# Performance work log

Measured on AMD Instinct MI355X. Metric: run time of the kernel, lower is better.

## Reference

```python
import jax, jax.numpy as jnp
import numpy as np

B, T, I, H, C = 1024, 256, 14, 128, 1


def setup_inputs() -> dict:
    key = jax.random.key(0)
    ks = jax.random.split(key, 12)
    s = 1.0 / np.sqrt(H)  # torch nn.LSTM / nn.Linear uniform init bound
    u = lambda k, shp: jax.random.uniform(k, shp, jnp.float32, -s, s)
    return {
        "x": jax.random.normal(ks[0], (B, T, I), jnp.float32),
        # layer 0 (input_size -> hidden), gate order i,f,g,o stacked along first dim (4H)
        "w_ih0": u(ks[1], (4 * H, I)), "w_hh0": u(ks[2], (4 * H, H)),
        "b_ih0": u(ks[3], (4 * H,)), "b_hh0": u(ks[4], (4 * H,)),
        # layer 1 (hidden -> hidden)
        "w_ih1": u(ks[5], (4 * H, H)), "w_hh1": u(ks[6], (4 * H, H)),
        "b_ih1": u(ks[7], (4 * H,)), "b_hh1": u(ks[8], (4 * H,)),
        # final linear head
        "w_lin": u(ks[9], (C, H)), "b_lin": u(ks[10], (C,)),
    }


def _lstm_layer(x_seq, w_ih, w_hh, b_ih, b_hh):
    """Single LSTM layer, batch_first input [B,T,D] -> hidden sequence [B,T,H]."""
    Bb = x_seq.shape[0]
    Hh = w_hh.shape[1]
    # Hoist the input projection out of the recurrence: one big GEMM over all timesteps.
    x_proj = jnp.einsum('btd,gd->btg', x_seq, w_ih) + b_ih + b_hh  # [B,T,4H]
    x_proj = jnp.swapaxes(x_proj, 0, 1)  # [T,B,4H] for scan over time
    h0 = jnp.zeros((Bb, Hh), x_seq.dtype)
    c0 = jnp.zeros((Bb, Hh), x_seq.dtype)

    def step(carry, xp):
        h, c = carry
        gates = xp + h @ w_hh.T  # [B,4H]
        i, f, g, o = jnp.split(gates, 4, axis=-1)  # torch gate order: i,f,g,o
        i = jax.nn.sigmoid(i)
        f = jax.nn.sigmoid(f)
        g = jnp.tanh(g)
        o = jax.nn.sigmoid(o)
        c = f * c + i * g
        h = o * jnp.tanh(c)
        return (h, c), h

    _, hs = jax.lax.scan(step, (h0, c0), x_proj)  # hs: [T,B,H]
    return jnp.swapaxes(hs, 0, 1)  # [B,T,H]


def reference(x, w_ih0, w_hh0, b_ih0, b_hh0, w_ih1, w_hh1, b_ih1, b_hh1, w_lin, b_lin):
    h1 = _lstm_layer(x, w_ih0, w_hh0, b_ih0, b_hh0)
    # nn.LSTM dropout=0.1 applies between layers only in training mode; inference => identity
    h2 = _lstm_layer(h1, w_ih1, w_hh1, b_ih1, b_hh1)
    last = h2[:, -1, :]  # [B,H] final timestep
    return last @ w_lin.T + b_lin  # [B,1]
```

## Files before the change

### kernel.cpp

```cpp
#include <hip/hip_runtime.h>

typedef _Float16 half8 __attribute__((ext_vector_type(8)));
typedef float floatx4 __attribute__((ext_vector_type(4)));

#define T_STEPS 256
#define BB      16
#define NTH     512
#define RING_W  16

#define WHH0_H  0
#define WIH1_H  65536
#define WHH1_H  131072
#define WIH0_H  196608
#define RING_H  229376
#define FLAG_B  4653056
#define FLAG_BYTES 16384

__device__ __forceinline__ float sig_(float z)  { return __builtin_amdgcn_rcpf(1.f + __expf(-z)); }
__device__ __forceinline__ float tanh_(float z) { return 1.f - 2.f * __builtin_amdgcn_rcpf(1.f + __expf(2.f * z)); }

__global__ __launch_bounds__(256) void prep_weights(
    const float* __restrict__ w_ih0, const float* __restrict__ w_hh0,
    const float* __restrict__ w_ih1, const float* __restrict__ w_hh1,
    _Float16* __restrict__ wf)
{
    const int idx = blockIdx.x * 256 + threadIdx.x;
    const int l  = idx & 63;
    const int ks = (idx >> 6) & 3;
    const int gi = (idx >> 8) & 3;
    const int wv = (idx >> 10) & 7;
    const int row = gi * 128 + wv * 16 + (l & 15);
    const int kb  = ks * 32 + (l >> 4) * 8;
#pragma unroll
    for (int j = 0; j < 8; ++j) {
        wf[WHH0_H + idx * 8 + j] = (_Float16)w_hh0[row * 128 + kb + j];
        wf[WIH1_H + idx * 8 + j] = (_Float16)w_ih1[row * 128 + kb + j];
        wf[WHH1_H + idx * 8 + j] = (_Float16)w_hh1[row * 128 + kb + j];
    }
    if (ks == 0) {
        const int lk = l >> 4;
        const int oi = ((wv * 4 + gi) * 64 + l) * 8;
#pragma unroll
        for (int j = 0; j < 8; ++j) {
            float v = 0.f;
            if (lk == 0)                v = w_ih0[row * 14 + j];
            else if (lk == 1 && j >= 2) v = w_ih0[row * 14 + 6 + j];
            wf[WIH0_H + oi + j] = (_Float16)v;
        }
    }
}

__global__ __launch_bounds__(NTH) void lstm2_pipe(
    const float* __restrict__ x, const _Float16* __restrict__ wf,
    const float* __restrict__ b_ih0, const float* __restrict__ b_hh0,
    const float* __restrict__ b_ih1, const float* __restrict__ b_hh1,
    const float* __restrict__ w_lin, const float* __restrict__ b_lin,
    float* __restrict__ out, char* __restrict__ wsb)
{
    __shared__ __align__(16) _Float16 hbuf[2][BB * 128];

    const int tid  = threadIdx.x;
    const int l    = tid & 63;
    const int wv   = tid >> 6;
    const int lrow = l & 15;
    const int lk   = l >> 4;
    const int bid  = blockIdx.x;
    const int pos  = bid & 7;
    const int role = (bid >> 3) & 1;
    const int g    = (bid >> 4) * 8 + pos;
    const int b0   = g * BB;

    _Float16* ring = (_Float16*)wsb + RING_H + (size_t)g * RING_W * 2048;
    int* flag_p = (int*)(wsb + FLAG_B) + g * 64;
    int* flag_c = flag_p + 32;

    for (int i = tid; i < 1024; i += NTH) ((unsigned*)hbuf[1])[i] = 0u;

    const half8* wsf = (const half8*)wf;

    if (role == 0) {
        half8 whh0f[16], wih0f[4];
#pragma unroll
        for (int gi = 0; gi < 4; ++gi) {
#pragma unroll
            for (int ks = 0; ks < 4; ++ks)
                whh0f[gi * 4 + ks] = wsf[WHH0_H / 8 + ((wv * 4 + gi) * 4 + ks) * 64 + l];
            wih0f[gi] = wsf[WIH0_H / 8 + (wv * 4 + gi) * 64 + l];
        }
        float bias1[4];
#pragma unroll
        for (int gi = 0; gi < 4; ++gi) {
            const int col = gi * 128 + wv * 16 + lrow;
            bias1[gi] = b_ih0[col] + b_hh0[col];
        }
        float c1[4] = {0.f, 0.f, 0.f, 0.f};

        const int coff = (lk == 1) ? 6 : 0;
        const float* xp = x + (size_t)(b0 + lrow) * (T_STEPS * 14) + coff;
        float xr[8];
#pragma unroll
        for (int j = 0; j < 8; ++j) xr[j] = xp[j];
        int seen_c = 0;
        __syncthreads();

        for (int t = 0; t < T_STEPS; ++t) {
            const int cur = t & 1, prv = cur ^ 1;
            half8 xh;
#pragma unroll
            for (int j = 0; j < 8; ++j) xh[j] = (_Float16)xr[j];
            if (t + 1 < T_STEPS) {
#pragma unroll
                for (int j = 0; j < 8; ++j) xr[j] = xp[(t + 1) * 14 + j];
            }
            const char* hrd = (const char*)hbuf[prv];
            half8 h1p[4];
#pragma unroll
            for (int ks = 0; ks < 4; ++ks) {
                const int off = lrow * 256 + ((ks * 64 + lk * 16) ^ ((lrow & 7) << 4));
                h1p[ks] = *(const half8*)(hrd + off);
            }
            floatx4 acc[4];
#pragma unroll
            for (int gi = 0; gi < 4; ++gi) {
                acc[gi] = (floatx4){bias1[gi], bias1[gi], bias1[gi], bias1[gi]};
                acc[gi] = __builtin_amdgcn_mfma_f32_16x16x32_f16(xh, wih0f[gi], acc[gi], 0, 0, 0);
#pragma unroll
                for (int ks = 0; ks < 4; ++ks)
                    acc[gi] = __builtin_amdgcn_mfma_f32_16x16x32_f16(h1p[ks], whh0f[gi * 4 + ks], acc[gi], 0, 0, 0);
            }
            if (t >= RING_W && tid == 0) {
                while (seen_c < t - (RING_W - 1)) {
                    seen_c = __hip_atomic_load(flag_c, __ATOMIC_RELAXED, __HIP_MEMORY_SCOPE_AGENT);
                    if (seen_c < t - (RING_W - 1)) __builtin_amdgcn_s_sleep(2);
                }
            }
            __syncthreads();
            char* hwr = (char*)hbuf[cur];
            _Float16* rt = ring + (size_t)(t & (RING_W - 1)) * 2048;
            const int u = wv * 16 + lrow;
#pragma unroll
            for (int r = 0; r < 4; ++r) {
                const float ig = sig_(acc[0][r]);
                const float fg = sig_(acc[1][r]);
                const float gg = tanh_(acc[2][r]);
                const float og = sig_(acc[3][r]);
                c1[r] = fg * c1[r] + ig * gg;
                const float hv = og * tanh_(c1[r]);
                const int b = lk * 4 + r;
                const _Float16 hh = (_Float16)hv;
                *(_Float16*)(hwr + b * 256 + ((u * 2) ^ ((b & 7) << 4))) = hh;
                rt[b * 128 + u] = hh;
            }
            __syncthreads();
            if (tid == 0)
                __hip_atomic_store(flag_p, t + 1, __ATOMIC_RELEASE, __HIP_MEMORY_SCOPE_AGENT);
        }
    } else {
        half8 wih1f[16], whh1f[16];
#pragma unroll
        for (int gi = 0; gi < 4; ++gi)
#pragma unroll
            for (int ks = 0; ks < 4; ++ks) {
                const int idx = ((wv * 4 + gi) * 4 + ks) * 64 + l;
                wih1f[gi * 4 + ks] = wsf[WIH1_H / 8 + idx];
                whh1f[gi * 4 + ks] = wsf[WHH1_H / 8 + idx];
            }
        float bias2[4];
#pragma unroll
        for (int gi = 0; gi < 4; ++gi) {
            const int col = gi * 128 + wv * 16 + lrow;
            bias2[gi] = b_ih1[col] + b_hh1[col];
        }
        float c2[4] = {0.f, 0.f, 0.f, 0.f};
        int seen_p = 0;
        const int toff = lrow * 128 + lk * 8;

        __syncthreads();
        if (tid == 0) {
            while (seen_p < 2) {
                seen_p = __hip_atomic_load(flag_p, __ATOMIC_ACQUIRE, __HIP_MEMORY_SCOPE_AGENT);
                if (seen_p < 2) __builtin_amdgcn_s_sleep(2);
            }
        }
        __syncthreads();
        half8 h1nA[4], h1nB[4];
#pragma unroll
        for (int ks = 0; ks < 4; ++ks) h1nA[ks] = *(const half8*)(ring + toff + ks * 32);
#pragma unroll
        for (int ks = 0; ks < 4; ++ks) h1nB[ks] = *(const half8*)(ring + 2048 + toff + ks * 32);

#define CSTEP(T, H1N, CUR)                                                          \
        {                                                                           \
            const char* hrd = (const char*)hbuf[(CUR) ^ 1];                         \
            half8 h2p[4];                                                           \
            _Pragma("unroll")                                                       \
            for (int ks = 0; ks < 4; ++ks) {                                        \
                const int off = lrow * 256 + ((ks * 64 + lk * 16) ^ ((lrow & 7) << 4)); \
                h2p[ks] = *(const half8*)(hrd + off);                               \
            }                                                                       \
            floatx4 acc[4];                                                         \
            _Pragma("unroll")                                                       \
            for (int gi = 0; gi < 4; ++gi) {                                        \
                acc[gi] = (floatx4){bias2[gi], bias2[gi], bias2[gi], bias2[gi]};    \
                _Pragma("unroll")                                                   \
                for (int ks = 0; ks < 4; ++ks) {                                    \
                    acc[gi] = __builtin_amdgcn_mfma_f32_16x16x32_f16(h2p[ks], whh1f[gi * 4 + ks], acc[gi], 0, 0, 0); \
                    acc[gi] = __builtin_amdgcn_mfma_f32_16x16x32_f16(H1N[ks], wih1f[gi * 4 + ks], acc[gi], 0, 0, 0); \
                }                                                                   \
            }                                                                       \
            char* hwr = (char*)hbuf[CUR];                                           \
            const int u = wv * 16 + lrow;                                           \
            _Pragma("unroll")                                                       \
            for (int r = 0; r < 4; ++r) {                                           \
                const float ig = sig_(acc[0][r]);                                   \
                const float fg = sig_(acc[1][r]);                                   \
                const float gg = tanh_(acc[2][r]);                                  \
                const float og = sig_(acc[3][r]);                                   \
                c2[r] = fg * c2[r] + ig * gg;                                       \
                const float hv = og * tanh_(c2[r]);                                 \
                const int b = lk * 4 + r;                                           \
                *(_Float16*)(hwr + b * 256 + ((u * 2) ^ ((b & 7) << 4))) = (_Float16)hv; \
            }                                                                       \
            if ((T) < T_STEPS - 2 && tid == 0) {                                    \
                while (seen_p < (T) + 3) {                                          \
                    seen_p = __hip_atomic_load(flag_p, __ATOMIC_ACQUIRE, __HIP_MEMORY_SCOPE_AGENT); \
                    if (seen_p < (T) + 3) __builtin_amdgcn_s_sleep(2);              \
                }                                                                   \
            }                                                                       \
            __syncthreads();                                                        \
            if ((T) < T_STEPS - 2) {                                                \
                const _Float16* rt = ring + (size_t)((((T) + 2) & (RING_W - 1))) * 2048; \
                _Pragma("unroll")                                                   \
                for (int ks = 0; ks < 4; ++ks)                                      \
                    H1N[ks] = *(const half8*)(rt + toff + ks * 32);                 \
            }                                                                       \
            if (tid == 0)                                                           \
                __hip_atomic_store(flag_c, (T) + 2, __ATOMIC_RELAXED, __HIP_MEMORY_SCOPE_AGENT); \
        }

        for (int t = 0; t < T_STEPS; t += 2) {
            CSTEP(t,     h1nA, 0);
            CSTEP(t + 1, h1nB, 1);
        }
#undef CSTEP

        if (tid < BB) {
            const char* hb = (const char*)hbuf[1];
            float acc = b_lin[0];
            for (int j = 0; j < 128; ++j) {
                const int off = tid * 256 + ((j * 2) ^ ((tid & 7) << 4));
                acc += w_lin[j] * (float)(*(const _Float16*)(hb + off));
            }
            out[b0 + tid] = acc;
        }
    }
}

extern "C" void kernel_launch(void* const* d_in, const int* in_sizes, int n_in,
                              void* d_out, int out_size, void* d_ws, size_t ws_size,
                              hipStream_t stream) {
    (void)in_sizes; (void)n_in; (void)ws_size; (void)out_size;
    const float* x     = (const float*)d_in[0];
    const float* w_ih0 = (const float*)d_in[1];
    const float* w_hh0 = (const float*)d_in[2];
    const float* b_ih0 = (const float*)d_in[3];
    const float* b_hh0 = (const float*)d_in[4];
    const float* w_ih1 = (const float*)d_in[5];
    const float* w_hh1 = (const float*)d_in[6];
    const float* b_ih1 = (const float*)d_in[7];
    const float* b_hh1 = (const float*)d_in[8];
    const float* w_lin = (const float*)d_in[9];
    const float* b_lin = (const float*)d_in[10];
    float* out = (float*)d_out;
    char* wsb = (char*)d_ws;

    hipMemsetAsync(wsb + FLAG_B, 0, FLAG_BYTES, stream);
    hipLaunchKernelGGL(prep_weights, dim3(32), dim3(256), 0, stream,
                       w_ih0, w_hh0, w_ih1, w_hh1, (_Float16*)d_ws);
    hipLaunchKernelGGL(lstm2_pipe, dim3(128), dim3(NTH), 0, stream,
                       x, (_Float16*)d_ws, b_ih0, b_hh0, b_ih1, b_hh1,
                       w_lin, b_lin, out, wsb);
}
```

Before: 545.8 us.

## Restructure producer/consumer LSTM sync: per-thread flag polling, split barriers, finer flags

Restructures the two-role LSTM pipeline's synchronisation. Every thread now polls the cross-block flags itself instead of thread 0 polling plus a __syncthreads, and each step uses one explicit waitcnt+s_barrier instead of two __syncthreads. The consumer publishes its progress flag every step and waits for producer data just before prefetching. The change also moves the x prefetch after the flag store, pins weight registers with empty asm, remaps block-to-role assignment, and parallelises the final linear head across 64 lanes with shuffles. It aims to cut barrier and polling latency on the serial recurrence, but many threads spinning on atomics raises memory traffic and the ring offsets change.

```diff
diff --git a/kernel.cpp b/kernel.cpp
--- a/kernel.cpp
+++ b/kernel.cpp
@@ -12,9 +12,9 @@
 #define WIH1_H  65536
 #define WHH1_H  131072
 #define WIH0_H  196608
-#define RING_H  229376
-#define FLAG_B  4653056
-#define FLAG_BYTES 16384
+#define RING_H  212992
+#define FLAG_B  4620288
+#define FLAG_BYTES 8192
 
 __device__ __forceinline__ float sig_(float z)  { return __builtin_amdgcn_rcpf(1.f + __expf(-z)); }
 __device__ __forceinline__ float tanh_(float z) { return 1.f - 2.f * __builtin_amdgcn_rcpf(1.f + __expf(2.f * z)); }
@@ -50,31 +50,40 @@
     }
 }
 
-__global__ __launch_bounds__(NTH) void lstm2_pipe(
+#define PIN(V) asm volatile("" : "+v"(V))
+
+#define READFRAG(DSTARR, SRC) do {                                              \
+    _Pragma("unroll")                                                           \
+    for (int ks = 0; ks < 4; ++ks) {                                            \
+        const int off = lrow * 256 + ((ks * 64 + lk * 16) ^ ((lrow & 7) << 4)); \
+        DSTARR[ks] = *(const half8*)((const char*)(SRC) + off);                 \
+    }                                                                           \
+} while (0)
+
+__global__ __launch_bounds__(NTH, 2) void lstm2_pipe2(
     const float* __restrict__ x, const _Float16* __restrict__ wf,
     const float* __restrict__ b_ih0, const float* __restrict__ b_hh0,
     const float* __restrict__ b_ih1, const float* __restrict__ b_hh1,
     const float* __restrict__ w_lin, const float* __restrict__ b_lin,
     float* __restrict__ out, char* __restrict__ wsb)
 {
-    __shared__ __align__(16) _Float16 hbuf[2][BB * 128];
+    __shared__ __align__(16) _Float16 hs[2][BB * 128];
 
     const int tid  = threadIdx.x;
     const int l    = tid & 63;
     const int wv   = tid >> 6;
     const int lrow = l & 15;
     const int lk   = l >> 4;
-    const int bid  = blockIdx.x;
-    const int pos  = bid & 7;
-    const int role = (bid >> 3) & 1;
-    const int g    = (bid >> 4) * 8 + pos;
+    const int g    = blockIdx.x & 63;
+    const int role = blockIdx.x >> 6;
     const int b0   = g * BB;
+    const int u    = wv * 16 + lrow;
 
     _Float16* ring = (_Float16*)wsb + RING_H + (size_t)g * RING_W * 2048;
-    int* flag_p = (int*)(wsb + FLAG_B) + g * 64;
-    int* flag_c = flag_p + 32;
-
-    for (int i = tid; i < 1024; i += NTH) ((unsigned*)hbuf[1])[i] = 0u;
+    int* fp = (int*)(wsb + FLAG_B) + g * 32;
+    int* fc = fp + 16;
+
+    for (int i = tid; i < 2048; i += NTH) ((unsigned*)hs)[i] = 0u;
 
     const half8* wsf = (const half8*)wf;
 
@@ -83,9 +92,12 @@
 #pragma unroll
         for (int gi = 0; gi < 4; ++gi) {
 #pragma unroll
-            for (int ks = 0; ks < 4; ++ks)
+            for (int ks = 0; ks < 4; ++ks) {
                 whh0f[gi * 4 + ks] = wsf[WHH0_H / 8 + ((wv * 4 + gi) * 4 + ks) * 64 + l];
+                PIN(whh0f[gi * 4 + ks]);
+            }
             wih0f[gi] = wsf[WIH0_H / 8 + (wv * 4 + gi) * 64 + l];
+            PIN(wih0f[gi]);
         }
         float bias1[4];
 #pragma unroll
@@ -94,7 +106,6 @@
             bias1[gi] = b_ih0[col] + b_hh0[col];
         }
         float c1[4] = {0.f, 0.f, 0.f, 0.f};
-
         const int coff = (lk == 1) ? 6 : 0;
         const float* xp = x + (size_t)(b0 + lrow) * (T_STEPS * 14) + coff;
         float xr[8];
@@ -108,17 +119,10 @@
             half8 xh;
 #pragma unroll
             for (int j = 0; j < 8; ++j) xh[j] = (_Float16)xr[j];
-            if (t + 1 < T_STEPS) {
-#pragma unroll
-                for (int j = 0; j < 8; ++j) xr[j] = xp[(t + 1) * 14 + j];
-            }
-            const char* hrd = (const char*)hbuf[prv];
+
             half8 h1p[4];
-#pragma unroll
-            for (int ks = 0; ks < 4; ++ks) {
-                const int off = lrow * 256 + ((ks * 64 + lk * 16) ^ ((lrow & 7) << 4));
-                h1p[ks] = *(const half8*)(hrd + off);
-            }
+            READFRAG(h1p, hs[prv]);
+
             floatx4 acc[4];
 #pragma unroll
             for (int gi = 0; gi < 4; ++gi) {
@@ -128,32 +132,40 @@
                 for (int ks = 0; ks < 4; ++ks)
                     acc[gi] = __builtin_amdgcn_mfma_f32_16x16x32_f16(h1p[ks], whh0f[gi * 4 + ks], acc[gi], 0, 0, 0);
             }
-            if (t >= RING_W && tid == 0) {
+
+            if (t >= RING_W) {
                 while (seen_c < t - (RING_W - 1)) {
-                    seen_c = __hip_atomic_load(flag_c, __ATOMIC_RELAXED, __HIP_MEMORY_SCOPE_AGENT);
+                    seen_c = __hip_atomic_load(fc, __ATOMIC_RELAXED, __HIP_MEMORY_SCOPE_AGENT);
                     if (seen_c < t - (RING_W - 1)) __builtin_amdgcn_s_sleep(2);
                 }
             }
-            __syncthreads();
-            char* hwr = (char*)hbuf[cur];
-            _Float16* rt = ring + (size_t)(t & (RING_W - 1)) * 2048;
-            const int u = wv * 16 + lrow;
-#pragma unroll
-            for (int r = 0; r < 4; ++r) {
-                const float ig = sig_(acc[0][r]);
-                const float fg = sig_(acc[1][r]);
-                const float gg = tanh_(acc[2][r]);
-                const float og = sig_(acc[3][r]);
-                c1[r] = fg * c1[r] + ig * gg;
-                const float hv = og * tanh_(c1[r]);
-                const int b = lk * 4 + r;
-                const _Float16 hh = (_Float16)hv;
-                *(_Float16*)(hwr + b * 256 + ((u * 2) ^ ((b & 7) << 4))) = hh;
-                rt[b * 128 + u] = hh;
-            }
-            __syncthreads();
+
+            {
+                char* hwr = (char*)hs[cur];
+                _Float16* rt = ring + (size_t)(t & (RING_W - 1)) * 2048;
+#pragma unroll
+                for (int r = 0; r < 4; ++r) {
+                    const float ig = sig_(acc[0][r]);
+                    const float fg = sig_(acc[1][r]);
+                    const float gg = tanh_(acc[2][r]);
+                    const float og = sig_(acc[3][r]);
+                    c1[r] = fg * c1[r] + ig * gg;
+                    const float hv = og * tanh_(c1[r]);
+                    const int b = lk * 4 + r;
+                    const _Float16 hh = (_Float16)hv;
+                    *(_Float16*)(hwr + b * 256 + ((u * 2) ^ ((b & 7) << 4))) = hh;
+                    rt[b * 128 + u] = hh;
+                }
+            }
+
+            asm volatile("s_waitcnt vmcnt(0) lgkmcnt(0)" ::: "memory");
+            __builtin_amdgcn_s_barrier();
             if (tid == 0)
-                __hip_atomic_store(flag_p, t + 1, __ATOMIC_RELEASE, __HIP_MEMORY_SCOPE_AGENT);
+                __hip_atomic_store(fp, t + 1, __ATOMIC_RELEASE, __HIP_MEMORY_SCOPE_AGENT);
+            if (t + 1 < T_STEPS) {
+#pragma unroll
+                for (int j = 0; j < 8; ++j) xr[j] = xp[(t + 1) * 14 + j];
+            }
         }
     } else {
         half8 wih1f[16], whh1f[16];
@@ -163,7 +175,9 @@
             for (int ks = 0; ks < 4; ++ks) {
                 const int idx = ((wv * 4 + gi) * 4 + ks) * 64 + l;
                 wih1f[gi * 4 + ks] = wsf[WIH1_H / 8 + idx];
+                PIN(wih1f[gi * 4 + ks]);
                 whh1f[gi * 4 + ks] = wsf[WHH1_H / 8 + idx];
+                PIN(whh1f[gi * 4 + ks]);
             }
         float bias2[4];
 #pragma unroll
@@ -173,31 +187,31 @@
         }
         float c2[4] = {0.f, 0.f, 0.f, 0.f};
         int seen_p = 0;
-        const int toff = lrow * 128 + lk * 8;
+        const int toff = lrow * 256 + lk * 16;
 
         __syncthreads();
-        if (tid == 0) {
-            while (seen_p < 2) {
-                seen_p = __hip_atomic_load(flag_p, __ATOMIC_ACQUIRE, __HIP_MEMORY_SCOPE_AGENT);
-                if (seen_p < 2) __builtin_amdgcn_s_sleep(2);
-            }
-        }
-        __syncthreads();
+
+#define WAITP(N) do {                                                               \
+        while (seen_p < (N)) {                                                      \
+            seen_p = __hip_atomic_load(fp, __ATOMIC_ACQUIRE, __HIP_MEMORY_SCOPE_AGENT); \
+            if (seen_p < (N)) __builtin_amdgcn_s_sleep(2);                          \
+        }                                                                           \
+    } while (0)
+
         half8 h1nA[4], h1nB[4];
-#pragma unroll
-        for (int ks = 0; ks < 4; ++ks) h1nA[ks] = *(const half8*)(ring + toff + ks * 32);
-#pragma unroll
-        for (int ks = 0; ks < 4; ++ks) h1nB[ks] = *(const half8*)(ring + 2048 + toff + ks * 32);
+        WAITP(1);
+#pragma unroll
+        for (int ks = 0; ks < 4; ++ks)
+            h1nA[ks] = *(const half8*)((const char*)ring + toff + ks * 64);
+        WAITP(2);
+#pragma unroll
+        for (int ks = 0; ks < 4; ++ks)
+            h1nB[ks] = *(const half8*)((const char*)ring + 4096 + toff + ks * 64);
 
 #define CSTEP(T, H1N, CUR)                                                          \
         {                                                                           \
-            const char* hrd = (const char*)hbuf[(CUR) ^ 1];                         \
             half8 h2p[4];                                                           \
-            _Pragma("unroll")                                                       \
-            for (int ks = 0; ks < 4; ++ks) {                                        \
-                const int off = lrow * 256 + ((ks * 64 + lk * 16) ^ ((lrow & 7) << 4)); \
-                h2p[ks] = *(const half8*)(hrd + off);                               \
-            }                                                                       \
+            READFRAG(h2p, hs[(CUR) ^ 1]);                                           \
             floatx4 acc[4];                                                         \
             _Pragma("unroll")                                                       \
             for (int gi = 0; gi < 4; ++gi) {                                        \
@@ -208,8 +222,7 @@
                     acc[gi] = __builtin_amdgcn_mfma_f32_16x16x32_f16(H1N[ks], wih1f[gi * 4 + ks], acc[gi], 0, 0, 0); \
                 }                                                                   \
             }                                                                       \
-            char* hwr = (char*)hbuf[CUR];                                           \
-            const int u = wv * 16 + lrow;                                           \
+            char* hwr = (char*)hs[CUR];                                             \
             _Pragma("unroll")                                                       \
             for (int r = 0; r < 4; ++r) {                                           \
                 const float ig = sig_(acc[0][r]);                                   \
@@ -221,21 +234,17 @@
                 const int b = lk * 4 + r;                                           \
                 *(_Float16*)(hwr + b * 256 + ((u * 2) ^ ((b & 7) << 4))) = (_Float16)hv; \
             }                                                                       \
-            if ((T) < T_STEPS - 2 && tid == 0) {                                    \
-                while (seen_p < (T) + 3) {                                          \
-                    seen_p = __hip_atomic_load(flag_p, __ATOMIC_ACQUIRE, __HIP_MEMORY_SCOPE_AGENT); \
-                    if (seen_p < (T) + 3) __builtin_amdgcn_s_sleep(2);              \
-                }                                                                   \
-            }                                                                       \
-            __syncthreads();                                                        \
+            asm volatile("s_waitcnt lgkmcnt(0)" ::: "memory");                      \
+            __builtin_amdgcn_s_barrier();                                           \
+            if (tid == 0)                                                           \
+                __hip_atomic_store(fc, (T) + 1, __ATOMIC_RELAXED, __HIP_MEMORY_SCOPE_AGENT); \
             if ((T) < T_STEPS - 2) {                                                \
-                const _Float16* rt = ring + (size_t)((((T) + 2) & (RING_W - 1))) * 2048; \
+                WAITP((T) + 3);                                                     \
+                const char* rt = (const char*)ring + (size_t)(((T) + 2) & (RING_W - 1)) * 4096; \
                 _Pragma("unroll")                                                   \
                 for (int ks = 0; ks < 4; ++ks)                                      \
-                    H1N[ks] = *(const half8*)(rt + toff + ks * 32);                 \
+                    H1N[ks] = *(const half8*)(rt + toff + ks * 64);                 \
             }                                                                       \
-            if (tid == 0)                                                           \
-                __hip_atomic_store(flag_c, (T) + 2, __ATOMIC_RELAXED, __HIP_MEMORY_SCOPE_AGENT); \
         }
 
         for (int t = 0; t < T_STEPS; t += 2) {
@@ -243,15 +252,20 @@
             CSTEP(t + 1, h1nB, 1);
         }
 #undef CSTEP
-
-        if (tid < BB) {
-            const char* hb = (const char*)hbuf[1];
-            float acc = b_lin[0];
-            for (int j = 0; j < 128; ++j) {
-                const int off = tid * 256 + ((j * 2) ^ ((tid & 7) << 4));
-                acc += w_lin[j] * (float)(*(const _Float16*)(hb + off));
-            }
-            out[b0 + tid] = acc;
+#undef WAITP
+
+        if (tid < 64) {
+            const char* hb = (const char*)hs[1];
+            const int bb = tid & 15, q = tid >> 4;
+            float acc = 0.f;
+#pragma unroll
+            for (int j5 = 0; j5 < 32; ++j5) {
+                const int j = q * 32 + j5;
+                acc += w_lin[j] * (float)(*(const _Float16*)(hb + bb * 256 + ((j * 2) ^ ((bb & 7) << 4))));
+            }
+            acc += __shfl_xor(acc, 16, 64);
+            acc += __shfl_xor(acc, 32, 64);
+            if (q == 0) out[b0 + bb] = acc + b_lin[0];
         }
     }
 }
@@ -277,7 +291,7 @@
     hipMemsetAsync(wsb + FLAG_B, 0, FLAG_BYTES, stream);
     hipLaunchKernelGGL(prep_weights, dim3(32), dim3(256), 0, stream,
                        w_ih0, w_hh0, w_ih1, w_hh1, (_Float16*)d_ws);
-    hipLaunchKernelGGL(lstm2_pipe, dim3(128), dim3(NTH), 0, stream,
-                       x, (_Float16*)d_ws, b_ih0, b_hh0, b_ih1, b_hh1,
+    hipLaunchKernelGGL(lstm2_pipe2, dim3(128), dim3(NTH), 0, stream,
+                       x, (const _Float16*)d_ws, b_ih0, b_hh0, b_ih1, b_hh1,
                        w_lin, b_lin, out, wsb);
 }
```

Measured after the change: 651.4 us. 19.4% more time.
